# Performance work log

Hardware: AMD Instinct MI355X
Metric: run time of the kernel (lower is better)

Reference implementation:

```python
import jax, jax.numpy as jnp
import numpy as np

B, L, D_MODEL = 2, 1024, 512
D_INNER, D_STATE, DT_RANK, D_CONV = 1024, 16, 32, 4
N_LAYER, VOCAB, EMBED_DIM, NUM_EMOTIONS = 2, 30000, 256, 7


def setup_inputs() -> dict:
    key = jax.random.key(0)
    ks = jax.random.split(key, 12)
    def n(k, shape, scale=0.02):
        return jax.random.normal(k, shape, jnp.float32) * scale
    A_init = jnp.broadcast_to(jnp.arange(1, D_STATE + 1, dtype=jnp.float32), (N_LAYER, D_INNER, D_STATE))
    return {
        "input_ids": jax.random.randint(ks[0], (B, L), 0, VOCAB),
        "embedding": n(ks[1], (VOCAB, D_MODEL)),
        "norm_w": jnp.ones((N_LAYER, D_MODEL)),
        "in_proj_w": n(ks[2], (N_LAYER, D_MODEL, 2 * D_INNER)),
        "conv_w": n(ks[3], (N_LAYER, D_INNER, 1, D_CONV), 0.1),
        "conv_b": jnp.zeros((N_LAYER, D_INNER)),
        "x_proj_w": n(ks[4], (N_LAYER, D_INNER, DT_RANK + 2 * D_STATE)),
        "dt_proj_w": n(ks[5], (N_LAYER, DT_RANK, D_INNER), 0.1),
        "dt_proj_b": jnp.zeros((N_LAYER, D_INNER)),
        "A_log": jnp.log(A_init),
        "D": jnp.ones((N_LAYER, D_INNER)),
        "out_proj_w": n(ks[6], (N_LAYER, D_INNER, D_MODEL)),
        "norm_f_w": jnp.ones((D_MODEL,)),
        "proj_w": n(ks[7], (D_MODEL, EMBED_DIM)),
        "proj_b": jnp.zeros((EMBED_DIM,)),
        "cls_w": n(ks[8], (EMBED_DIM, NUM_EMOTIONS)),
        "cls_b": jnp.zeros((NUM_EMOTIONS,)),
    }


def rmsnorm(x, w, eps=1e-5):
    return x * jax.lax.rsqrt(jnp.mean(x * x, axis=-1, keepdims=True) + eps) * w


def selective_scan(u, delta, A, B_, C, D_):
    # u, delta: [b,l,d]; A: [d,n]; B_, C: [b,l,n]; D_: [d]
    dA = jnp.exp(jnp.einsum('bld,dn->bldn', delta, A))          # [b,l,d,n]
    dBu = jnp.einsum('bld,bln,bld->bldn', delta, B_, u)          # [b,l,d,n]
    def step(h, inp):
        dA_t, dBu_t, C_t = inp                                   # [b,d,n],[b,d,n],[b,n]
        h = dA_t * h + dBu_t
        y = jnp.einsum('bdn,bn->bd', h, C_t)
        return h, y
    h0 = jnp.zeros((u.shape[0], u.shape[2], A.shape[1]), u.dtype)
    _, ys = jax.lax.scan(step, h0, (dA.transpose(1, 0, 2, 3), dBu.transpose(1, 0, 2, 3), C.transpose(1, 0, 2)))
    return ys.transpose(1, 0, 2) + u * D_                        # [b,l,d]


def mamba_block(x, in_w, cw, cb, xp_w, dt_w, dt_b, A_log, D_, out_w):
    # x: [b,l,d_model]
    xr = x @ in_w                                                # [b,l,2*d_inner]
    xi, res = jnp.split(xr, 2, axis=-1)
    # causal depthwise conv1d over time
    xc = jax.lax.conv_general_dilated(
        xi.transpose(0, 2, 1), cw, window_strides=(1,),
        padding=[(D_CONV - 1, 0)], feature_group_count=D_INNER,
        dimension_numbers=('NCH', 'OIH', 'NCH'))
    xi = jax.nn.silu(xc.transpose(0, 2, 1) + cb)                 # [b,l,d_inner]
    x_dbl = xi @ xp_w
    delta, B_, C = jnp.split(x_dbl, [DT_RANK, DT_RANK + D_STATE], axis=-1)
    delta = jax.nn.softplus(delta @ dt_w + dt_b)                 # [b,l,d_inner]
    A = -jnp.exp(A_log)
    y = selective_scan(xi, delta, A, B_, C, D_)
    y = y * jax.nn.silu(res)
    return y @ out_w                                             # [b,l,d_model]


def reference(input_ids, embedding, norm_w, in_proj_w, conv_w, conv_b, x_proj_w,
              dt_proj_w, dt_proj_b, A_log, D, out_proj_w, norm_f_w,
              proj_w, proj_b, cls_w, cls_b):
    x = embedding[input_ids]                                     # [b,l,d_model]
    for i in range(N_LAYER):
        x = x + mamba_block(rmsnorm(x, norm_w[i]), in_proj_w[i], conv_w[i],
                            conv_b[i], x_proj_w[i], dt_proj_w[i], dt_proj_b[i],
                            A_log[i], D[i], out_proj_w[i])
    x = rmsnorm(x, norm_f_w)
    pooled = x.mean(axis=1)                                      # [b,d_model]
    emotion_emb = pooled @ proj_w + proj_b                       # [b,embed_dim]
    logits = emotion_emb @ cls_w + cls_b                         # [b,num_emotions]
    return logits, emotion_emb
```

## Files before the change

### kernel.cpp

```cpp
#include <hip/hip_runtime.h>
#include <cstddef>

#define D_MODEL   512
#define D_INNER   1024
#define D_STATE   16
#define DT_RANK   32
#define SEQ_L     1024
#define BATCH     2
#define NLAYER    2
#define M_ROWS    (BATCH * SEQ_L)
#define NC        32
#define LC        (SEQ_L / NC)

typedef __bf16 bf16x8 __attribute__((ext_vector_type(8)));
typedef float  f32x4  __attribute__((ext_vector_type(4)));

__device__ __forceinline__ float softplus_f(float x) {
    return fmaxf(x, 0.f) + log1pf(expf(-fabsf(x)));
}
__device__ __forceinline__ float silu_f(float x) {
    return x / (1.f + __expf(-x));
}
__device__ __forceinline__ unsigned short f2bf(float f) {
    unsigned u = __float_as_uint(f);
    return (unsigned short)((u + 0x7fffu + ((u >> 16) & 1u)) >> 16);
}
__device__ __forceinline__ unsigned pack_bf2(float lo, float hi) {
    return (unsigned)f2bf(lo) | ((unsigned)f2bf(hi) << 16);
}

__global__ void embed_kernel(const int* __restrict__ ids,
                             const float* __restrict__ emb,
                             float* __restrict__ x) {
    int g = blockIdx.x * blockDim.x + threadIdx.x;
    int c = (g & 127) << 2;
    int m = g >> 7;
    int row = ids[m];
    *(float4*)&x[(size_t)m * D_MODEL + c] =
        *(const float4*)&emb[(size_t)row * D_MODEL + c];
}

__global__ __launch_bounds__(64) void rmsnorm_bf_kernel(const float* __restrict__ x,
                                                        const float* __restrict__ w,
                                                        unsigned short* __restrict__ out) {
    int row = blockIdx.x;
    int tid = threadIdx.x;
    const float* xp = x + (size_t)row * D_MODEL;
    float4 v0 = *(const float4*)&xp[tid * 4];
    float4 v1 = *(const float4*)&xp[256 + tid * 4];
    float ss = v0.x*v0.x + v0.y*v0.y + v0.z*v0.z + v0.w*v0.w
             + v1.x*v1.x + v1.y*v1.y + v1.z*v1.z + v1.w*v1.w;
    #pragma unroll
    for (int off = 32; off > 0; off >>= 1) ss += __shfl_xor(ss, off);
    float scale = rsqrtf(ss * (1.f / D_MODEL) + 1e-5f);
    float4 w0 = *(const float4*)&w[tid * 4];
    float4 w1 = *(const float4*)&w[256 + tid * 4];
    unsigned short* op = out + (size_t)row * D_MODEL;
    uint2 p0, p1;
    p0.x = pack_bf2(v0.x * scale * w0.x, v0.y * scale * w0.y);
    p0.y = pack_bf2(v0.z * scale * w0.z, v0.w * scale * w0.w);
    p1.x = pack_bf2(v1.x * scale * w1.x, v1.y * scale * w1.y);
    p1.y = pack_bf2(v1.z * scale * w1.z, v1.w * scale * w1.w);
    *(uint2*)&op[tid * 4] = p0;
    *(uint2*)&op[256 + tid * 4] = p1;
}

__global__ __launch_bounds__(256) void castT_kernel(const float* __restrict__ W,
                                                    unsigned short* __restrict__ Wt,
                                                    int K, int N) {
    __shared__ float tile[32][33];
    int n0 = blockIdx.x * 32, k0 = blockIdx.y * 32;
    int tx = threadIdx.x & 31, ty = threadIdx.x >> 5;
    #pragma unroll
    for (int i = 0; i < 4; ++i)
        tile[ty + i*8][tx] = W[(size_t)(k0 + ty + i*8) * N + n0 + tx];
    __syncthreads();
    #pragma unroll
    for (int i = 0; i < 4; ++i)
        Wt[(size_t)(n0 + ty + i*8) * K + k0 + tx] = f2bf(tile[tx][ty + i*8]);
}

template<int EPI>
__global__ __launch_bounds__(256) void gemm_mfma(const unsigned short* __restrict__ A,
                                                 const unsigned short* __restrict__ Bt,
                                                 float* __restrict__ C,
                                                 int K, int ldc) {
    __shared__ unsigned short As[64 * 64];
    __shared__ unsigned short Bs[64 * 64];
    int m0 = blockIdx.y * 64;
    int n0 = blockIdx.x * 64;
    int t = threadIdx.x;
    int lane = t & 63, wave = t >> 6;
    int wr = wave >> 1, wc = wave & 1;
    int srow = t >> 3;
    int sc8  = t & 7;
    f32x4 acc[2][2] = {};

    for (int k0 = 0; k0 < K; k0 += 64) {
        __syncthreads();
        #pragma unroll
        for (int i = 0; i < 2; ++i) {
            int row = i * 32 + srow;
            int csrc = sc8 ^ (row & 7);
            __builtin_amdgcn_global_load_lds(
                (const __attribute__((address_space(1))) void*)
                    &A[(size_t)(m0 + row) * K + k0 + csrc * 8],
                (__attribute__((address_space(3))) void*)
                    &As[row * 64 + sc8 * 8], 16, 0, 0);
            __builtin_amdgcn_global_load_lds(
                (const __attribute__((address_space(1))) void*)
                    &Bt[(size_t)(n0 + row) * K + k0 + csrc * 8],
                (__attribute__((address_space(3))) void*)
                    &Bs[row * 64 + sc8 * 8], 16, 0, 0);
        }
        __syncthreads();
        #pragma unroll
        for (int ks = 0; ks < 2; ++ks) {
            bf16x8 av[2], bv[2];
            #pragma unroll
            for (int f = 0; f < 2; ++f) {
                int ar = wr * 32 + f * 16 + (lane & 15);
                int ac = (ks * 4 + (lane >> 4)) ^ (ar & 7);
                av[f] = *reinterpret_cast<const bf16x8*>(&As[ar * 64 + ac * 8]);
                int br = wc * 32 + f * 16 + (lane & 15);
                int bc = (ks * 4 + (lane >> 4)) ^ (br & 7);
                bv[f] = *reinterpret_cast<const bf16x8*>(&Bs[br * 64 + bc * 8]);
            }
            #pragma unroll
            for (int fm = 0; fm < 2; ++fm)
                #pragma unroll
                for (int fn = 0; fn < 2; ++fn)
                    acc[fm][fn] = __builtin_amdgcn_mfma_f32_16x16x32_bf16(
                        av[fm], bv[fn], acc[fm][fn], 0, 0, 0);
        }
    }
    #pragma unroll
    for (int fm = 0; fm < 2; ++fm)
        #pragma unroll
        for (int fn = 0; fn < 2; ++fn) {
            int row = m0 + wr * 32 + fm * 16 + (lane >> 4) * 4;
            int col = n0 + wc * 32 + fn * 16 + (lane & 15);
            #pragma unroll
            for (int r = 0; r < 4; ++r) {
                float* cp = &C[(size_t)(row + r) * ldc + col];
                if (EPI == 2) *cp += acc[fm][fn][r]; else *cp = acc[fm][fn][r];
            }
        }
}

__global__ void conv_silu_kernel(const float* __restrict__ xr,
                                 const float* __restrict__ cw,
                                 const float* __restrict__ cb,
                                 float* __restrict__ out) {
    int g = blockIdx.x * blockDim.x + threadIdx.x;
    int d = g & (D_INNER - 1);
    int m = g >> 10;
    int l = m & (SEQ_L - 1);
    float4 w = *(const float4*)&cw[d * 4];
    const float* col = &xr[(size_t)m * 2048 + d];
    float x3 = col[0];
    float x2 = (l >= 1) ? col[-2048] : 0.f;
    float x1 = (l >= 2) ? col[-4096] : 0.f;
    float x0 = (l >= 3) ? col[-6144] : 0.f;
    float acc = cb[d] + w.x * x0 + w.y * x1 + w.z * x2 + w.w * x3;
    out[g] = silu_f(acc);
}

__global__ __launch_bounds__(256) void xproj_kernel(const float* __restrict__ A,
                                                    const float* __restrict__ Bw,
                                                    float* __restrict__ Cc) {
    __shared__ float Bsh[64][68];
    __shared__ float Ash[4][64];
    int row0 = blockIdx.x * 4;
    int t = threadIdx.x;
    int tr = t >> 6, c = t & 63;
    int kk = t >> 2, cb4 = (t & 3) << 4;
    float acc = 0.f;
    for (int k0 = 0; k0 < 1024; k0 += 64) {
        __syncthreads();
        #pragma unroll
        for (int j = 0; j < 4; ++j) {
            float4 v = *(const float4*)&Bw[(size_t)(k0 + kk) * 64 + cb4 + j * 4];
            *(float4*)&Bsh[kk][cb4 + j * 4] = v;
        }
        Ash[tr][c] = A[(size_t)(row0 + tr) * 1024 + k0 + c];
        __syncthreads();
        #pragma unroll
        for (int k = 0; k < 64; ++k)
            acc = fmaf(Ash[tr][k], Bsh[k][c], acc);
    }
    Cc[(size_t)(row0 + tr) * 64 + c] = acc;
}

#define BM 64
#define BN 64
#define BKK 16
__global__ __launch_bounds__(256) void gemm_dt(const float* __restrict__ A,
                                               const float* __restrict__ Bm,
                                               const float* __restrict__ bias,
                                               float* __restrict__ C,
                                               int lda, int ldb, int ldc) {
    __shared__ float As[BM][BKK + 4];
    __shared__ float Bs[BKK][BN];
    int tid = threadIdx.x;
    int n0 = blockIdx.x * BN;
    int m0 = blockIdx.y * BM;
    int tx4 = (tid & 15) << 2;
    int ty4 = (tid >> 4) << 2;
    int arow = tid >> 2, akk = (tid & 3) << 2;
    int brow = tid >> 4, bcol = (tid & 15) << 2;
    float acc[4][4] = {};
    for (int k0 = 0; k0 < 32; k0 += BKK) {
        float4 av = *(const float4*)&A[(size_t)(m0 + arow) * lda + k0 + akk];
        float4 bv = *(const float4*)&Bm[(size_t)(k0 + brow) * ldb + n0 + bcol];
        *(float4*)&As[arow][akk] = av;
        *(float4*)&Bs[brow][bcol] = bv;
        __syncthreads();
        #pragma unroll
        for (int k = 0; k < BKK; ++k) {
            float a0 = As[ty4 + 0][k];
            float a1 = As[ty4 + 1][k];
            float a2 = As[ty4 + 2][k];
            float a3 = As[ty4 + 3][k];
            float4 b = *(float4*)&Bs[k][tx4];
            acc[0][0] = fmaf(a0, b.x, acc[0][0]); acc[0][1] = fmaf(a0, b.y, acc[0][1]);
            acc[0][2] = fmaf(a0, b.z, acc[0][2]); acc[0][3] = fmaf(a0, b.w, acc[0][3]);
            acc[1][0] = fmaf(a1, b.x, acc[1][0]); acc[1][1] = fmaf(a1, b.y, acc[1][1]);
            acc[1][2] = fmaf(a1, b.z, acc[1][2]); acc[1][3] = fmaf(a1, b.w, acc[1][3]);
            acc[2][0] = fmaf(a2, b.x, acc[2][0]); acc[2][1] = fmaf(a2, b.y, acc[2][1]);
            acc[2][2] = fmaf(a2, b.z, acc[2][2]); acc[2][3] = fmaf(a2, b.w, acc[2][3]);
            acc[3][0] = fmaf(a3, b.x, acc[3][0]); acc[3][1] = fmaf(a3, b.y, acc[3][1]);
            acc[3][2] = fmaf(a3, b.z, acc[3][2]); acc[3][3] = fmaf(a3, b.w, acc[3][3]);
        }
        __syncthreads();
    }
    #pragma unroll
    for (int i = 0; i < 4; ++i) {
        int m = m0 + ty4 + i;
        float4 bb = *(const float4*)&bias[n0 + tx4];
        float4 v = make_float4(softplus_f(acc[i][0] + bb.x), softplus_f(acc[i][1] + bb.y),
                               softplus_f(acc[i][2] + bb.z), softplus_f(acc[i][3] + bb.w));
        *(float4*)&C[(size_t)m * ldc + n0 + tx4] = v;
    }
}

__global__ __launch_bounds__(256) void scan_p1(const float* __restrict__ u_,
                                               const float* __restrict__ delta,
                                               const float* __restrict__ xdbl,
                                               const float* __restrict__ A_log,
                                               float* __restrict__ aprod,
                                               float* __restrict__ hloc) {
    int d = blockIdx.x * 256 + threadIdx.x;
    int b = blockIdx.y;
    int c = blockIdx.z;
    int l0 = c * LC;
    __shared__ float sB[LC][D_STATE];
    for (int i = threadIdx.x; i < LC * D_STATE; i += 256) {
        int l = i >> 4, n = i & 15;
        sB[l][n] = xdbl[((size_t)(b * SEQ_L + l0 + l)) * 64 + DT_RANK + n];
    }
    __syncthreads();
    float A_[D_STATE], h[D_STATE], ap[D_STATE];
    #pragma unroll
    for (int n = 0; n < D_STATE; ++n) {
        A_[n] = -__expf(A_log[(size_t)d * D_STATE + n]);
        h[n] = 0.f; ap[n] = 1.f;
    }
    for (int l = 0; l < LC; ++l) {
        size_t m = (size_t)b * SEQ_L + l0 + l;
        float dt = delta[m * D_INNER + d];
        float uu = u_[m * D_INNER + d];
        float du = dt * uu;
        #pragma unroll
        for (int n = 0; n < D_STATE; ++n) {
            float e = __expf(dt * A_[n]);
            h[n] = fmaf(e, h[n], du * sB[l][n]);
            ap[n] *= e;
        }
    }
    #pragma unroll
    for (int n = 0; n < D_STATE; ++n) {
        size_t o = (((size_t)b * NC + c) * D_STATE + n) * D_INNER + d;
        aprod[o] = ap[n];
        hloc[o] = h[n];
    }
}

__global__ __launch_bounds__(256) void scan_p2(const float* __restrict__ aprod,
                                               float* __restrict__ hloc) {
    int d = blockIdx.x * 256 + threadIdx.x;
    int n = blockIdx.y;
    int b = blockIdx.z;
    float h = 0.f;
    for (int c = 0; c < NC; ++c) {
        size_t o = (((size_t)b * NC + c) * D_STATE + n) * D_INNER + d;
        float ap = aprod[o];
        float lc = hloc[o];
        hloc[o] = h;
        h = fmaf(ap, h, lc);
    }
}

__global__ __launch_bounds__(256) void scan_p3(const float* __restrict__ u_,
                                               const float* __restrict__ delta,
                                               const float* __restrict__ xdbl,
                                               const float* __restrict__ A_log,
                                               const float* __restrict__ Dp,
                                               const float* __restrict__ hinit,
                                               const float* __restrict__ xr,
                                               unsigned short* __restrict__ y) {
    int d = blockIdx.x * 256 + threadIdx.x;
    int b = blockIdx.y;
    int c = blockIdx.z;
    int l0 = c * LC;
    __shared__ float sBC[LC][2 * D_STATE];
    for (int i = threadIdx.x; i < LC * 2 * D_STATE; i += 256) {
        int l = i >> 5, j = i & 31;
        sBC[l][j] = xdbl[((size_t)(b * SEQ_L + l0 + l)) * 64 + DT_RANK + j];
    }
    __syncthreads();
    float A_[D_STATE], h[D_STATE];
    #pragma unroll
    for (int n = 0; n < D_STATE; ++n) {
        A_[n] = -__expf(A_log[(size_t)d * D_STATE + n]);
        size_t o = (((size_t)b * NC + c) * D_STATE + n) * D_INNER + d;
        h[n] = hinit[o];
    }
    float Dd = Dp[d];
    for (int l = 0; l < LC; ++l) {
        size_t m = (size_t)b * SEQ_L + l0 + l;
        float dt = delta[m * D_INNER + d];
        float uu = u_[m * D_INNER + d];
        float du = dt * uu;
        float yv = 0.f;
        #pragma unroll
        for (int n = 0; n < D_STATE; ++n) {
            float e = __expf(dt * A_[n]);
            h[n] = fmaf(e, h[n], du * sBC[l][n]);
            yv = fmaf(h[n], sBC[l][D_STATE + n], yv);
        }
        yv = fmaf(uu, Dd, yv);
        float res = xr[m * 2048 + 1024 + d];
        y[m * D_INNER + d] = f2bf(yv * silu_f(res));
    }
}

__global__ __launch_bounds__(256) void rms_pool1(const float* __restrict__ x,
                                                 float* __restrict__ partial) {
    int blk = blockIdx.x;
    int b = blk >> 5, c = blk & 31;
    int wave = threadIdx.x >> 6, lane = threadIdx.x & 63;
    int row0 = b * SEQ_L + c * 32 + wave * 8;
    float4 a0 = make_float4(0.f, 0.f, 0.f, 0.f);
    float4 a1 = make_float4(0.f, 0.f, 0.f, 0.f);
    for (int r = 0; r < 8; ++r) {
        const float* xp = x + (size_t)(row0 + r) * D_MODEL;
        float4 v0 = *(const float4*)&xp[lane * 4];
        float4 v1 = *(const float4*)&xp[256 + lane * 4];
        float ss = v0.x*v0.x + v0.y*v0.y + v0.z*v0.z + v0.w*v0.w
                 + v1.x*v1.x + v1.y*v1.y + v1.z*v1.z + v1.w*v1.w;
        #pragma unroll
        for (int off = 32; off > 0; off >>= 1) ss += __shfl_xor(ss, off);
        float s = rsqrtf(ss * (1.f / D_MODEL) + 1e-5f);
        a0.x = fmaf(v0.x, s, a0.x); a0.y = fmaf(v0.y, s, a0.y);
        a0.z = fmaf(v0.z, s, a0.z); a0.w = fmaf(v0.w, s, a0.w);
        a1.x = fmaf(v1.x, s, a1.x); a1.y = fmaf(v1.y, s, a1.y);
        a1.z = fmaf(v1.z, s, a1.z); a1.w = fmaf(v1.w, s, a1.w);
    }
    __shared__ float red[4][512];
    *(float4*)&red[wave][lane * 4] = a0;
    *(float4*)&red[wave][256 + lane * 4] = a1;
    __syncthreads();
    int d = threadIdx.x * 2;
    float s0 = red[0][d] + red[1][d] + red[2][d] + red[3][d];
    float s1 = red[0][d+1] + red[1][d+1] + red[2][d+1] + red[3][d+1];
    partial[(size_t)blk * 512 + d]     = s0;
    partial[(size_t)blk * 512 + d + 1] = s1;
}

__global__ __launch_bounds__(512) void pool2_kernel(const float* __restrict__ partial,
                                                    const float* __restrict__ w,
                                                    float* __restrict__ pooled) {
    int b = blockIdx.x, d = threadIdx.x;
    float s = 0.f;
    #pragma unroll
    for (int c = 0; c < 32; ++c)
        s += partial[((size_t)b * 32 + c) * 512 + d];
    pooled[b * 512 + d] = s * (1.f / SEQ_L) * w[d];
}

__global__ __launch_bounds__(256) void embp1_kernel(const float* __restrict__ pooled,
                                                    const float* __restrict__ pw,
                                                    float* __restrict__ partial) {
    int b = blockIdx.x, kc = blockIdx.y;
    int e = threadIdx.x;
    float acc = 0.f;
    #pragma unroll 8
    for (int i = 0; i < 64; ++i) {
        int k = kc * 64 + i;
        acc = fmaf(pooled[b * 512 + k], pw[(size_t)k * 256 + e], acc);
    }
    partial[((size_t)b * 8 + kc) * 256 + e] = acc;
}

__global__ __launch_bounds__(512) void embp2_kernel(const float* __restrict__ partial,
                                                    const float* __restrict__ pb,
                                                    float* __restrict__ out14) {
    int t = threadIdx.x;
    int b = t >> 8, e = t & 255;
    float s = pb[e];
    #pragma unroll
    for (int kc = 0; kc < 8; ++kc)
        s += partial[((size_t)b * 8 + kc) * 256 + e];
    out14[b * 256 + e] = s;
}

__global__ __launch_bounds__(896) void logits_kernel(const float* __restrict__ embv,
                                                     const float* __restrict__ cw,
                                                     const float* __restrict__ cb,
                                                     float* __restrict__ out) {
    int wave = threadIdx.x >> 6, lane = threadIdx.x & 63;
    int b = wave / 7, c = wave % 7;
    float acc = 0.f;
    #pragma unroll
    for (int i = 0; i < 4; ++i) {
        int k = lane + i * 64;
        acc = fmaf(embv[b * 256 + k], cw[k * 7 + c], acc);
    }
    #pragma unroll
    for (int off = 32; off > 0; off >>= 1) acc += __shfl_xor(acc, off);
    if (lane == 0) out[b * 7 + c] = acc + cb[c];
}

extern "C" void kernel_launch(void* const* d_in, const int* in_sizes, int n_in,
                              void* d_out, int out_size, void* d_ws, size_t ws_size,
                              hipStream_t stream) {
    const int*   ids    = (const int*)d_in[0];
    const float* emb    = (const float*)d_in[1];
    const float* norm_w = (const float*)d_in[2];
    const float* in_w   = (const float*)d_in[3];
    const float* conv_w = (const float*)d_in[4];
    const float* conv_b = (const float*)d_in[5];
    const float* xp_w   = (const float*)d_in[6];
    const float* dt_w   = (const float*)d_in[7];
    const float* dt_b   = (const float*)d_in[8];
    const float* A_log  = (const float*)d_in[9];
    const float* Dp     = (const float*)d_in[10];
    const float* out_w  = (const float*)d_in[11];
    const float* normf  = (const float*)d_in[12];
    const float* proj_w = (const float*)d_in[13];
    const float* proj_b = (const float*)d_in[14];
    const float* cls_w  = (const float*)d_in[15];
    const float* cls_b  = (const float*)d_in[16];
    float* out = (float*)d_out;

    float* ws     = (float*)d_ws;
    float* x      = ws;
    float* xn     = x + 1048576;
    float* xr     = xn + 1048576;
    float* xconv  = xr + 4194304;
    float* xdbl   = xconv + 2097152;
    float* delta  = xdbl + 131072;
    float* yb     = delta + 2097152;
    float* pooled = yb + 2097152;
    float* eparts = pooled + 1024;

    float* aprod  = yb;
    float* hloc   = xn;
    float* ppart  = xn;
    unsigned short* in_wt  = (unsigned short*)delta;
    unsigned short* xn_bf  = (unsigned short*)(delta + 524288);
    unsigned short* out_wt = (unsigned short*)xconv;
    unsigned short* yb_bf  = (unsigned short*)(yb + 1048576);

    embed_kernel<<<1024, 256, 0, stream>>>(ids, emb, x);

    for (int i = 0; i < NLAYER; ++i) {
        castT_kernel<<<dim3(64, 16), 256, 0, stream>>>(
            in_w + (size_t)i * D_MODEL * 2 * D_INNER, in_wt, 512, 2048);
        rmsnorm_bf_kernel<<<M_ROWS, 64, 0, stream>>>(x, norm_w + i * D_MODEL, xn_bf);
        gemm_mfma<0><<<dim3(2048 / 64, M_ROWS / 64), 256, 0, stream>>>(
            xn_bf, in_wt, xr, 512, 2048);
        conv_silu_kernel<<<(M_ROWS * D_INNER) / 256, 256, 0, stream>>>(
            xr, conv_w + i * D_INNER * 4, conv_b + i * D_INNER, xconv);
        xproj_kernel<<<M_ROWS / 4, 256, 0, stream>>>(
            xconv, xp_w + (size_t)i * D_INNER * 64, xdbl);
        gemm_dt<<<dim3(1024 / BN, M_ROWS / BM), 256, 0, stream>>>(
            xdbl, dt_w + (size_t)i * DT_RANK * D_INNER, dt_b + i * D_INNER, delta,
            64, 1024, 1024);

        scan_p1<<<dim3(D_INNER / 256, BATCH, NC), 256, 0, stream>>>(
            xconv, delta, xdbl, A_log + (size_t)i * D_INNER * D_STATE, aprod, hloc);
        scan_p2<<<dim3(D_INNER / 256, D_STATE, BATCH), 256, 0, stream>>>(
            aprod, hloc);
        scan_p3<<<dim3(D_INNER / 256, BATCH, NC), 256, 0, stream>>>(
            xconv, delta, xdbl, A_log + (size_t)i * D_INNER * D_STATE,
            Dp + (size_t)i * D_INNER, hloc, xr, yb_bf);

        castT_kernel<<<dim3(16, 32), 256, 0, stream>>>(
            out_w + (size_t)i * D_INNER * D_MODEL, out_wt, 1024, 512);
        gemm_mfma<2><<<dim3(512 / 64, M_ROWS / 64), 256, 0, stream>>>(
            yb_bf, out_wt, x, 1024, 512);
    }

    rms_pool1<<<BATCH * 32, 256, 0, stream>>>(x, ppart);
    pool2_kernel<<<BATCH, 512, 0, stream>>>(ppart, normf, pooled);
    embp1_kernel<<<dim3(BATCH, 8), 256, 0, stream>>>(pooled, proj_w, eparts);
    embp2_kernel<<<1, 512, 0, stream>>>(eparts, proj_b, out + 14);
    logits_kernel<<<1, 896, 0, stream>>>(out + 14, cls_w, cls_b, out);
}
```

Before: 260.9 us.

## Fuse conv/silu and dt projection into scan, store in_proj output as bf16

The in_proj GEMM now writes bf16 instead of fp32. The depthwise conv and SiLU are folded into the x_proj kernel and recomputed inside both scan passes. The dt low-rank projection and softplus are also computed inside the scan kernels, using a shared-memory copy of the dt weights, so the xconv and delta buffers are no longer materialised. Weight transposes are batched across layers into two launches, and the head kernels are merged from four into two. This cuts global memory traffic and launch count, at the cost of redundant conv and dt arithmetic in the scan passes and bf16 precision on xr and the residual gate.

```diff
diff --git a/kernel.cpp b/kernel.cpp
--- a/kernel.cpp
+++ b/kernel.cpp
@@ -24,6 +24,9 @@
 __device__ __forceinline__ unsigned short f2bf(float f) {
     unsigned u = __float_as_uint(f);
     return (unsigned short)((u + 0x7fffu + ((u >> 16) & 1u)) >> 16);
+}
+__device__ __forceinline__ float bf2f(unsigned short v) {
+    return __uint_as_float(((unsigned)v) << 16);
 }
 __device__ __forceinline__ unsigned pack_bf2(float lo, float hi) {
     return (unsigned)f2bf(lo) | ((unsigned)f2bf(hi) << 16);
@@ -68,6 +71,8 @@
 __global__ __launch_bounds__(256) void castT_kernel(const float* __restrict__ W,
                                                     unsigned short* __restrict__ Wt,
                                                     int K, int N) {
+    W  += (size_t)blockIdx.z * K * N;
+    Wt += (size_t)blockIdx.z * K * N;
     __shared__ float tile[32][33];
     int n0 = blockIdx.x * 32, k0 = blockIdx.y * 32;
     int tx = threadIdx.x & 31, ty = threadIdx.x >> 5;
@@ -84,6 +89,7 @@
 __global__ __launch_bounds__(256) void gemm_mfma(const unsigned short* __restrict__ A,
                                                  const unsigned short* __restrict__ Bt,
                                                  float* __restrict__ C,
+                                                 unsigned short* __restrict__ Cb,
                                                  int K, int ldc) {
     __shared__ unsigned short As[64 * 64];
     __shared__ unsigned short Bs[64 * 64];
@@ -142,39 +148,24 @@
             int col = n0 + wc * 32 + fn * 16 + (lane & 15);
             #pragma unroll
             for (int r = 0; r < 4; ++r) {
-                float* cp = &C[(size_t)(row + r) * ldc + col];
-                if (EPI == 2) *cp += acc[fm][fn][r]; else *cp = acc[fm][fn][r];
+                if (EPI == 2) C[(size_t)(row + r) * ldc + col] += acc[fm][fn][r];
+                else          Cb[(size_t)(row + r) * ldc + col] = f2bf(acc[fm][fn][r]);
             }
         }
 }
 
-__global__ void conv_silu_kernel(const float* __restrict__ xr,
-                                 const float* __restrict__ cw,
-                                 const float* __restrict__ cb,
-                                 float* __restrict__ out) {
-    int g = blockIdx.x * blockDim.x + threadIdx.x;
-    int d = g & (D_INNER - 1);
-    int m = g >> 10;
-    int l = m & (SEQ_L - 1);
-    float4 w = *(const float4*)&cw[d * 4];
-    const float* col = &xr[(size_t)m * 2048 + d];
-    float x3 = col[0];
-    float x2 = (l >= 1) ? col[-2048] : 0.f;
-    float x1 = (l >= 2) ? col[-4096] : 0.f;
-    float x0 = (l >= 3) ? col[-6144] : 0.f;
-    float acc = cb[d] + w.x * x0 + w.y * x1 + w.z * x2 + w.w * x3;
-    out[g] = silu_f(acc);
-}
-
-__global__ __launch_bounds__(256) void xproj_kernel(const float* __restrict__ A,
-                                                    const float* __restrict__ Bw,
-                                                    float* __restrict__ Cc) {
+__global__ __launch_bounds__(256) void xproj_f(const unsigned short* __restrict__ xi,
+                                               const float* __restrict__ cw,
+                                               const float* __restrict__ cb,
+                                               const float* __restrict__ Bw,
+                                               float* __restrict__ Cc) {
     __shared__ float Bsh[64][68];
     __shared__ float Ash[4][64];
     int row0 = blockIdx.x * 4;
     int t = threadIdx.x;
     int tr = t >> 6, c = t & 63;
     int kk = t >> 2, cb4 = (t & 3) << 4;
+    int l = (row0 + tr) & (SEQ_L - 1);
     float acc = 0.f;
     for (int k0 = 0; k0 < 1024; k0 += 64) {
         __syncthreads();
@@ -183,7 +174,16 @@
             float4 v = *(const float4*)&Bw[(size_t)(k0 + kk) * 64 + cb4 + j * 4];
             *(float4*)&Bsh[kk][cb4 + j * 4] = v;
         }
-        Ash[tr][c] = A[(size_t)(row0 + tr) * 1024 + k0 + c];
+        {
+            int d = k0 + c;
+            float4 w = *(const float4*)&cw[d * 4];
+            const unsigned short* col = &xi[(size_t)(row0 + tr) * 2048 + d];
+            float x3 = bf2f(col[0]);
+            float x2 = (l >= 1) ? bf2f(col[-2048]) : 0.f;
+            float x1 = (l >= 2) ? bf2f(col[-4096]) : 0.f;
+            float x0 = (l >= 3) ? bf2f(col[-6144]) : 0.f;
+            Ash[tr][c] = silu_f(cb[d] + w.x*x0 + w.y*x1 + w.z*x2 + w.w*x3);
+        }
         __syncthreads();
         #pragma unroll
         for (int k = 0; k < 64; ++k)
@@ -192,72 +192,27 @@
     Cc[(size_t)(row0 + tr) * 64 + c] = acc;
 }
 
-#define BM 64
-#define BN 64
-#define BKK 16
-__global__ __launch_bounds__(256) void gemm_dt(const float* __restrict__ A,
-                                               const float* __restrict__ Bm,
-                                               const float* __restrict__ bias,
-                                               float* __restrict__ C,
-                                               int lda, int ldb, int ldc) {
-    __shared__ float As[BM][BKK + 4];
-    __shared__ float Bs[BKK][BN];
+__global__ __launch_bounds__(256) void scan_p1f(const unsigned short* __restrict__ xi,
+                                                const float* __restrict__ xdbl,
+                                                const float* __restrict__ dtw,
+                                                const float* __restrict__ dtb_,
+                                                const float* __restrict__ cw,
+                                                const float* __restrict__ cb,
+                                                const float* __restrict__ A_log,
+                                                float* __restrict__ aprod,
+                                                float* __restrict__ hloc) {
     int tid = threadIdx.x;
-    int n0 = blockIdx.x * BN;
-    int m0 = blockIdx.y * BM;
-    int tx4 = (tid & 15) << 2;
-    int ty4 = (tid >> 4) << 2;
-    int arow = tid >> 2, akk = (tid & 3) << 2;
-    int brow = tid >> 4, bcol = (tid & 15) << 2;
-    float acc[4][4] = {};
-    for (int k0 = 0; k0 < 32; k0 += BKK) {
-        float4 av = *(const float4*)&A[(size_t)(m0 + arow) * lda + k0 + akk];
-        float4 bv = *(const float4*)&Bm[(size_t)(k0 + brow) * ldb + n0 + bcol];
-        *(float4*)&As[arow][akk] = av;
-        *(float4*)&Bs[brow][bcol] = bv;
-        __syncthreads();
-        #pragma unroll
-        for (int k = 0; k < BKK; ++k) {
-            float a0 = As[ty4 + 0][k];
-            float a1 = As[ty4 + 1][k];
-            float a2 = As[ty4 + 2][k];
-            float a3 = As[ty4 + 3][k];
-            float4 b = *(float4*)&Bs[k][tx4];
-            acc[0][0] = fmaf(a0, b.x, acc[0][0]); acc[0][1] = fmaf(a0, b.y, acc[0][1]);
-            acc[0][2] = fmaf(a0, b.z, acc[0][2]); acc[0][3] = fmaf(a0, b.w, acc[0][3]);
-            acc[1][0] = fmaf(a1, b.x, acc[1][0]); acc[1][1] = fmaf(a1, b.y, acc[1][1]);
-            acc[1][2] = fmaf(a1, b.z, acc[1][2]); acc[1][3] = fmaf(a1, b.w, acc[1][3]);
-            acc[2][0] = fmaf(a2, b.x, acc[2][0]); acc[2][1] = fmaf(a2, b.y, acc[2][1]);
-            acc[2][2] = fmaf(a2, b.z, acc[2][2]); acc[2][3] = fmaf(a2, b.w, acc[2][3]);
-            acc[3][0] = fmaf(a3, b.x, acc[3][0]); acc[3][1] = fmaf(a3, b.y, acc[3][1]);
-            acc[3][2] = fmaf(a3, b.z, acc[3][2]); acc[3][3] = fmaf(a3, b.w, acc[3][3]);
-        }
-        __syncthreads();
-    }
-    #pragma unroll
-    for (int i = 0; i < 4; ++i) {
-        int m = m0 + ty4 + i;
-        float4 bb = *(const float4*)&bias[n0 + tx4];
-        float4 v = make_float4(softplus_f(acc[i][0] + bb.x), softplus_f(acc[i][1] + bb.y),
-                               softplus_f(acc[i][2] + bb.z), softplus_f(acc[i][3] + bb.w));
-        *(float4*)&C[(size_t)m * ldc + n0 + tx4] = v;
-    }
-}
-
-__global__ __launch_bounds__(256) void scan_p1(const float* __restrict__ u_,
-                                               const float* __restrict__ delta,
-                                               const float* __restrict__ xdbl,
-                                               const float* __restrict__ A_log,
-                                               float* __restrict__ aprod,
-                                               float* __restrict__ hloc) {
-    int d = blockIdx.x * 256 + threadIdx.x;
-    int b = blockIdx.y;
-    int c = blockIdx.z;
+    int d = blockIdx.x * 256 + tid;
+    int b = blockIdx.y, c = blockIdx.z;
     int l0 = c * LC;
-    __shared__ float sB[LC][D_STATE];
-    for (int i = threadIdx.x; i < LC * D_STATE; i += 256) {
-        int l = i >> 4, n = i & 15;
-        sB[l][n] = xdbl[((size_t)(b * SEQ_L + l0 + l)) * 64 + DT_RANK + n];
+    __shared__ float sX[LC][64];
+    __shared__ float sW[32][256];
+    #pragma unroll
+    for (int k = 0; k < 32; ++k)
+        sW[k][tid] = dtw[k * 1024 + blockIdx.x * 256 + tid];
+    for (int i = tid; i < LC * 64; i += 256) {
+        int l = i >> 6, j = i & 63;
+        sX[l][j] = xdbl[(size_t)(b * SEQ_L + l0 + l) * 64 + j];
     }
     __syncthreads();
     float A_[D_STATE], h[D_STATE], ap[D_STATE];
@@ -266,15 +221,25 @@
         A_[n] = -__expf(A_log[(size_t)d * D_STATE + n]);
         h[n] = 0.f; ap[n] = 1.f;
     }
+    float4 w = *(const float4*)&cw[d * 4];
+    float cbd = cb[d], dtb = dtb_[d];
+    const unsigned short* xcol = xi + (size_t)(b * SEQ_L + l0) * 2048 + d;
+    float t1 = (l0 >= 1) ? bf2f(xcol[-2048]) : 0.f;
+    float t2 = (l0 >= 2) ? bf2f(xcol[-4096]) : 0.f;
+    float t3 = (l0 >= 3) ? bf2f(xcol[-6144]) : 0.f;
     for (int l = 0; l < LC; ++l) {
-        size_t m = (size_t)b * SEQ_L + l0 + l;
-        float dt = delta[m * D_INNER + d];
-        float uu = u_[m * D_INNER + d];
-        float du = dt * uu;
+        float dtv = dtb;
+        #pragma unroll
+        for (int k = 0; k < 32; ++k) dtv = fmaf(sX[l][k], sW[k][tid], dtv);
+        dtv = softplus_f(dtv);
+        float t0 = bf2f(xcol[l * 2048]);
+        float uu = silu_f(cbd + w.x*t3 + w.y*t2 + w.z*t1 + w.w*t0);
+        t3 = t2; t2 = t1; t1 = t0;
+        float du = dtv * uu;
         #pragma unroll
         for (int n = 0; n < D_STATE; ++n) {
-            float e = __expf(dt * A_[n]);
-            h[n] = fmaf(e, h[n], du * sB[l][n]);
+            float e = __expf(dtv * A_[n]);
+            h[n] = fmaf(e, h[n], du * sX[l][32 + n]);
             ap[n] *= e;
         }
     }
@@ -301,22 +266,28 @@
     }
 }
 
-__global__ __launch_bounds__(256) void scan_p3(const float* __restrict__ u_,
-                                               const float* __restrict__ delta,
-                                               const float* __restrict__ xdbl,
-                                               const float* __restrict__ A_log,
-                                               const float* __restrict__ Dp,
-                                               const float* __restrict__ hinit,
-                                               const float* __restrict__ xr,
-                                               unsigned short* __restrict__ y) {
-    int d = blockIdx.x * 256 + threadIdx.x;
-    int b = blockIdx.y;
-    int c = blockIdx.z;
+__global__ __launch_bounds__(256) void scan_p3f(const unsigned short* __restrict__ xi,
+                                                const float* __restrict__ xdbl,
+                                                const float* __restrict__ dtw,
+                                                const float* __restrict__ dtb_,
+                                                const float* __restrict__ cw,
+                                                const float* __restrict__ cb,
+                                                const float* __restrict__ A_log,
+                                                const float* __restrict__ Dp,
+                                                const float* __restrict__ hinit,
+                                                unsigned short* __restrict__ y) {
+    int tid = threadIdx.x;
+    int d = blockIdx.x * 256 + tid;
+    int b = blockIdx.y, c = blockIdx.z;
     int l0 = c * LC;
-    __shared__ float sBC[LC][2 * D_STATE];
-    for (int i = threadIdx.x; i < LC * 2 * D_STATE; i += 256) {
-        int l = i >> 5, j = i & 31;
-        sBC[l][j] = xdbl[((size_t)(b * SEQ_L + l0 + l)) * 64 + DT_RANK + j];
+    __shared__ float sX[LC][64];
+    __shared__ float sW[32][256];
+    #pragma unroll
+    for (int k = 0; k < 32; ++k)
+        sW[k][tid] = dtw[k * 1024 + blockIdx.x * 256 + tid];
+    for (int i = tid; i < LC * 64; i += 256) {
+        int l = i >> 6, j = i & 63;
+        sX[l][j] = xdbl[(size_t)(b * SEQ_L + l0 + l) * 64 + j];
     }
     __syncthreads();
     float A_[D_STATE], h[D_STATE];
@@ -327,21 +298,31 @@
         h[n] = hinit[o];
     }
     float Dd = Dp[d];
+    float4 w = *(const float4*)&cw[d * 4];
+    float cbd = cb[d], dtb = dtb_[d];
+    const unsigned short* xcol = xi + (size_t)(b * SEQ_L + l0) * 2048 + d;
+    float t1 = (l0 >= 1) ? bf2f(xcol[-2048]) : 0.f;
+    float t2 = (l0 >= 2) ? bf2f(xcol[-4096]) : 0.f;
+    float t3 = (l0 >= 3) ? bf2f(xcol[-6144]) : 0.f;
     for (int l = 0; l < LC; ++l) {
-        size_t m = (size_t)b * SEQ_L + l0 + l;
-        float dt = delta[m * D_INNER + d];
-        float uu = u_[m * D_INNER + d];
-        float du = dt * uu;
+        float dtv = dtb;
+        #pragma unroll
+        for (int k = 0; k < 32; ++k) dtv = fmaf(sX[l][k], sW[k][tid], dtv);
+        dtv = softplus_f(dtv);
+        float t0 = bf2f(xcol[l * 2048]);
+        float uu = silu_f(cbd + w.x*t3 + w.y*t2 + w.z*t1 + w.w*t0);
+        t3 = t2; t2 = t1; t1 = t0;
+        float du = dtv * uu;
         float yv = 0.f;
         #pragma unroll
         for (int n = 0; n < D_STATE; ++n) {
-            float e = __expf(dt * A_[n]);
-            h[n] = fmaf(e, h[n], du * sBC[l][n]);
-            yv = fmaf(h[n], sBC[l][D_STATE + n], yv);
+            float e = __expf(dtv * A_[n]);
+            h[n] = fmaf(e, h[n], du * sX[l][32 + n]);
+            yv = fmaf(h[n], sX[l][48 + n], yv);
         }
         yv = fmaf(uu, Dd, yv);
-        float res = xr[m * 2048 + 1024 + d];
-        y[m * D_INNER + d] = f2bf(yv * silu_f(res));
+        float res = bf2f(xcol[l * 2048 + 1024]);
+        y[(size_t)(b * SEQ_L + l0 + l) * D_INNER + d] = f2bf(yv * silu_f(res));
     }
 }
 
@@ -378,58 +359,59 @@
     partial[(size_t)blk * 512 + d + 1] = s1;
 }
 
-__global__ __launch_bounds__(512) void pool2_kernel(const float* __restrict__ partial,
-                                                    const float* __restrict__ w,
-                                                    float* __restrict__ pooled) {
-    int b = blockIdx.x, d = threadIdx.x;
-    float s = 0.f;
-    #pragma unroll
-    for (int c = 0; c < 32; ++c)
-        s += partial[((size_t)b * 32 + c) * 512 + d];
-    pooled[b * 512 + d] = s * (1.f / SEQ_L) * w[d];
-}
-
-__global__ __launch_bounds__(256) void embp1_kernel(const float* __restrict__ pooled,
-                                                    const float* __restrict__ pw,
-                                                    float* __restrict__ partial) {
+__global__ __launch_bounds__(256) void embp1f(const float* __restrict__ ppart,
+                                              const float* __restrict__ w,
+                                              const float* __restrict__ pw,
+                                              float* __restrict__ partial) {
     int b = blockIdx.x, kc = blockIdx.y;
-    int e = threadIdx.x;
+    int t = threadIdx.x;
+    __shared__ float sp[64];
+    if (t < 64) {
+        int dd = kc * 64 + t;
+        float s = 0.f;
+        #pragma unroll
+        for (int c = 0; c < 32; ++c)
+            s += ppart[((size_t)b * 32 + c) * 512 + dd];
+        sp[t] = s * (1.f / SEQ_L) * w[dd];
+    }
+    __syncthreads();
     float acc = 0.f;
     #pragma unroll 8
     for (int i = 0; i < 64; ++i) {
         int k = kc * 64 + i;
-        acc = fmaf(pooled[b * 512 + k], pw[(size_t)k * 256 + e], acc);
-    }
-    partial[((size_t)b * 8 + kc) * 256 + e] = acc;
-}
-
-__global__ __launch_bounds__(512) void embp2_kernel(const float* __restrict__ partial,
-                                                    const float* __restrict__ pb,
-                                                    float* __restrict__ out14) {
+        acc = fmaf(sp[i], pw[(size_t)k * 256 + t], acc);
+    }
+    partial[((size_t)b * 8 + kc) * 256 + t] = acc;
+}
+
+__global__ __launch_bounds__(512) void head_kernel(const float* __restrict__ eparts,
+                                                   const float* __restrict__ pb,
+                                                   const float* __restrict__ cw,
+                                                   const float* __restrict__ cb,
+                                                   float* __restrict__ out) {
+    __shared__ float se[2][256];
     int t = threadIdx.x;
     int b = t >> 8, e = t & 255;
     float s = pb[e];
     #pragma unroll
     for (int kc = 0; kc < 8; ++kc)
-        s += partial[((size_t)b * 8 + kc) * 256 + e];
-    out14[b * 256 + e] = s;
-}
-
-__global__ __launch_bounds__(896) void logits_kernel(const float* __restrict__ embv,
-                                                     const float* __restrict__ cw,
-                                                     const float* __restrict__ cb,
-                                                     float* __restrict__ out) {
-    int wave = threadIdx.x >> 6, lane = threadIdx.x & 63;
-    int b = wave / 7, c = wave % 7;
-    float acc = 0.f;
-    #pragma unroll
-    for (int i = 0; i < 4; ++i) {
-        int k = lane + i * 64;
-        acc = fmaf(embv[b * 256 + k], cw[k * 7 + c], acc);
-    }
-    #pragma unroll
-    for (int off = 32; off > 0; off >>= 1) acc += __shfl_xor(acc, off);
-    if (lane == 0) out[b * 7 + c] = acc + cb[c];
+        s += eparts[((size_t)b * 8 + kc) * 256 + e];
+    out[14 + b * 256 + e] = s;
+    se[b][e] = s;
+    __syncthreads();
+    int wave = t >> 6, lane = t & 63;
+    for (int idx = wave; idx < 14; idx += 8) {
+        int bb = idx / 7, cc = idx % 7;
+        float a = 0.f;
+        #pragma unroll
+        for (int i = 0; i < 4; ++i) {
+            int k = lane + i * 64;
+            a = fmaf(se[bb][k], cw[k * 7 + cc], a);
+        }
+        #pragma unroll
+        for (int off = 32; off > 0; off >>= 1) a += __shfl_xor(a, off);
+        if (lane == 0) out[bb * 7 + cc] = a + cb[cc];
+    }
 }
 
 extern "C" void kernel_launch(void* const* d_in, const int* in_sizes, int n_in,
@@ -458,54 +440,50 @@
     float* x      = ws;
     float* xn     = x + 1048576;
     float* xr     = xn + 1048576;
-    float* xconv  = xr + 4194304;
-    float* xdbl   = xconv + 2097152;
-    float* delta  = xdbl + 131072;
-    float* yb     = delta + 2097152;
-    float* pooled = yb + 2097152;
-    float* eparts = pooled + 1024;
-
-    float* aprod  = yb;
-    float* hloc   = xn;
-    float* ppart  = xn;
-    unsigned short* in_wt  = (unsigned short*)delta;
-    unsigned short* xn_bf  = (unsigned short*)(delta + 524288);
-    unsigned short* out_wt = (unsigned short*)xconv;
+    float* xconvR = xr + 4194304;
+    float* xdbl   = xconvR + 2097152;
+    float* wreg   = xdbl + 131072;
+    float* yb     = wreg + 2097152;
+    float* eparts = yb + 2097152 + 1024;
+
+    unsigned short* xn_bf  = (unsigned short*)xn;
+    float*          hloc   = xn;
+    float*          ppart  = xn;
+    unsigned short* xr_bf  = (unsigned short*)xr;
+    unsigned short* in_wt_all  = (unsigned short*)wreg;
+    unsigned short* out_wt_all = (unsigned short*)(wreg + 1048576);
+    float*          aprod  = yb;
     unsigned short* yb_bf  = (unsigned short*)(yb + 1048576);
 
     embed_kernel<<<1024, 256, 0, stream>>>(ids, emb, x);
+    castT_kernel<<<dim3(64, 16, NLAYER), 256, 0, stream>>>(in_w, in_wt_all, 512, 2048);
+    castT_kernel<<<dim3(16, 32, NLAYER), 256, 0, stream>>>(out_w, out_wt_all, 1024, 512);
 
     for (int i = 0; i < NLAYER; ++i) {
-        castT_kernel<<<dim3(64, 16), 256, 0, stream>>>(
-            in_w + (size_t)i * D_MODEL * 2 * D_INNER, in_wt, 512, 2048);
+        unsigned short* in_wt  = in_wt_all  + (size_t)i * 2048 * 512;
+        unsigned short* out_wt = out_wt_all + (size_t)i * 512 * 1024;
+        const float* cwi = conv_w + (size_t)i * D_INNER * 4;
+        const float* cbi = conv_b + (size_t)i * D_INNER;
+        const float* dtwi = dt_w + (size_t)i * DT_RANK * D_INNER;
+        const float* dtbi = dt_b + (size_t)i * D_INNER;
+        const float* Ali  = A_log + (size_t)i * D_INNER * D_STATE;
+
         rmsnorm_bf_kernel<<<M_ROWS, 64, 0, stream>>>(x, norm_w + i * D_MODEL, xn_bf);
-        gemm_mfma<0><<<dim3(2048 / 64, M_ROWS / 64), 256, 0, stream>>>(
-            xn_bf, in_wt, xr, 512, 2048);
-        conv_silu_kernel<<<(M_ROWS * D_INNER) / 256, 256, 0, stream>>>(
-            xr, conv_w + i * D_INNER * 4, conv_b + i * D_INNER, xconv);
-        xproj_kernel<<<M_ROWS / 4, 256, 0, stream>>>(
-            xconv, xp_w + (size_t)i * D_INNER * 64, xdbl);
-        gemm_dt<<<dim3(1024 / BN, M_ROWS / BM), 256, 0, stream>>>(
-            xdbl, dt_w + (size_t)i * DT_RANK * D_INNER, dt_b + i * D_INNER, delta,
-            64, 1024, 1024);
-
-        scan_p1<<<dim3(D_INNER / 256, BATCH, NC), 256, 0, stream>>>(
-            xconv, delta, xdbl, A_log + (size_t)i * D_INNER * D_STATE, aprod, hloc);
-        scan_p2<<<dim3(D_INNER / 256, D_STATE, BATCH), 256, 0, stream>>>(
-            aprod, hloc);
-        scan_p3<<<dim3(D_INNER / 256, BATCH, NC), 256, 0, stream>>>(
-            xconv, delta, xdbl, A_log + (size_t)i * D_INNER * D_STATE,
-            Dp + (size_t)i * D_INNER, hloc, xr, yb_bf);
-
-        castT_kernel<<<dim3(16, 32), 256, 0, stream>>>(
-            out_w + (size_t)i * D_INNER * D_MODEL, out_wt, 1024, 512);
-        gemm_mfma<2><<<dim3(512 / 64, M_ROWS / 64), 256, 0, stream>>>(
-            yb_bf, out_wt, x, 1024, 512);
+        gemm_mfma<3><<<dim3(32, 32), 256, 0, stream>>>(
+            xn_bf, in_wt, nullptr, xr_bf, 512, 2048);
+        xproj_f<<<M_ROWS / 4, 256, 0, stream>>>(
+            xr_bf, cwi, cbi, xp_w + (size_t)i * D_INNER * 64, xdbl);
+        scan_p1f<<<dim3(4, BATCH, NC), 256, 0, stream>>>(
+            xr_bf, xdbl, dtwi, dtbi, cwi, cbi, Ali, aprod, hloc);
+        scan_p2<<<dim3(4, D_STATE, BATCH), 256, 0, stream>>>(aprod, hloc);
+        scan_p3f<<<dim3(4, BATCH, NC), 256, 0, stream>>>(
+            xr_bf, xdbl, dtwi, dtbi, cwi, cbi, Ali,
+            Dp + (size_t)i * D_INNER, hloc, yb_bf);
+        gemm_mfma<2><<<dim3(8, 32), 256, 0, stream>>>(
+            yb_bf, out_wt, x, nullptr, 1024, 512);
     }
 
     rms_pool1<<<BATCH * 32, 256, 0, stream>>>(x, ppart);
-    pool2_kernel<<<BATCH, 512, 0, stream>>>(ppart, normf, pooled);
-    embp1_kernel<<<dim3(BATCH, 8), 256, 0, stream>>>(pooled, proj_w, eparts);
-    embp2_kernel<<<1, 512, 0, stream>>>(eparts, proj_b, out + 14);
-    logits_kernel<<<1, 896, 0, stream>>>(out + 14, cls_w, cls_b, out);
-}
+    embp1f<<<dim3(BATCH, 8), 256, 0, stream>>>(ppart, normf, proj_w, eparts);
+    head_kernel<<<1, 512, 0, stream>>>(eparts, proj_b, cls_w, cls_b, out);
+}
```

New measurement: 268.7 us. +3.0%, slower.
